# Optimization experiments

Measured on AMD Instinct MI355X. Metric: run time of the kernel, lower is better.

## Reference

```python
import jax, jax.numpy as jnp
import numpy as np

K = 16          # knn neighbors (init kwarg k)
GROUPS = 4      # GroupNorm groups
EPS = 1e-5
SLOPE = 0.2     # LeakyReLU negative slope


def fps(xyz, n):
    """Farthest point sampling. xyz: (B,N,3) -> idx (B,n). First index is 0 (pointnet2 convention)."""
    B, N, _ = xyz.shape

    def step(carry, _):
        dist, last = carry
        p = jnp.take_along_axis(xyz, last[:, None, None], axis=1)  # (B,1,3)
        d = jnp.sum((xyz - p) ** 2, axis=-1)                       # (B,N)
        dist = jnp.minimum(dist, d)
        nxt = jnp.argmax(dist, axis=-1).astype(jnp.int32)
        return (dist, nxt), nxt

    init = (jnp.full((B, N), jnp.inf, xyz.dtype), jnp.zeros((B,), jnp.int32))
    _, idxs = jax.lax.scan(step, init, None, length=n - 1)  # (n-1, B)
    return jnp.concatenate([jnp.zeros((B, 1), jnp.int32), idxs.T], axis=1)


def graph_feature(cq, fq, ck, fk):
    """DGCNN edge features. cq:(B,Q,3) fq:(B,Q,C) ck:(B,N,3) fk:(B,N,C) -> (B,Q,K,2C)."""
    d2 = (jnp.sum(cq * cq, -1)[:, :, None]
          - 2.0 * jnp.einsum('bqc,bnc->bqn', cq, ck)
          + jnp.sum(ck * ck, -1)[:, None, :])        # (B,Q,N)
    _, idx = jax.lax.top_k(-d2, K)                    # (B,Q,K) nearest first
    nb = jax.vmap(lambda f_, i_: f_[i_])(fk, idx)     # (B,Q,K,C)
    ctr = jnp.broadcast_to(fq[:, :, None, :], nb.shape)
    return jnp.concatenate([nb - ctr, ctr], axis=-1)


def conv_gn_lrelu(y, W, gw, gb):
    """1x1 Conv2d (no bias) + GroupNorm(4) + LeakyReLU(0.2). y: (B,Q,K,Cin), W: (Cout,Cin)."""
    y = jnp.einsum('bqkc,oc->bqko', y, W)
    B, Q, Kk, C = y.shape
    yg = y.reshape(B, Q * Kk, GROUPS, C // GROUPS)
    m = yg.mean(axis=(1, 3), keepdims=True)
    v = yg.var(axis=(1, 3), keepdims=True)
    y = ((yg - m) * jax.lax.rsqrt(v + EPS)).reshape(B, Q, Kk, C) * gw + gb
    return jnp.where(y > 0, y, SLOPE * y)


def setup_inputs() -> dict:
    key = jax.random.key(0)
    ks = jax.random.split(key, 16)
    B, N = 8, 4096
    s = lambda k_, shape, scale=0.1: (jax.random.normal(k_, shape, jnp.float32) * scale)
    return {
        'x': jax.random.normal(ks[0], (B, N, 7), jnp.float32),
        'W_in': s(ks[1], (8, 3), 0.5), 'b_in': s(ks[2], (8,), 0.02),
        'W1': s(ks[3], (32, 16), 0.2), 'g1w': jnp.ones((32,), jnp.float32), 'g1b': jnp.zeros((32,), jnp.float32),
        'W2': s(ks[4], (64, 64), 0.1), 'g2w': jnp.ones((64,), jnp.float32), 'g2b': jnp.zeros((64,), jnp.float32),
        'W3': s(ks[5], (64, 128), 0.1), 'g3w': jnp.ones((64,), jnp.float32), 'g3b': jnp.zeros((64,), jnp.float32),
        'W4': s(ks[6], (128, 128), 0.1), 'g4w': jnp.ones((128,), jnp.float32), 'g4b': jnp.zeros((128,), jnp.float32),
        'num0': 1024,
    }


def reference(x, W_in, b_in, W1, g1w, g1b, W2, g2w, g2b, W3, g3w, g3b, W4, g4w, g4b, num0):
    coor, normal, plane = x[..., :3], x[..., 3:6], x[..., 6:7]   # (B,N,3),(B,N,3),(B,N,1)

    # input_trans: Conv1d(3,8,1)
    f = jnp.einsum('bnc,oc->bno', coor, W_in) + b_in             # (B,N,8)

    g = graph_feature(coor, f, coor, f)                          # (B,N,K,16)
    f = conv_gn_lrelu(g, W1, g1w, g1b).max(axis=2)               # (B,N,32)

    idx = fps(coor, num0)
    gather = lambda a: jnp.take_along_axis(a, idx[:, :, None], axis=1)
    coor_q, normal_q, plane_q, f_q = gather(coor), gather(normal), gather(plane), gather(f)

    g = graph_feature(coor_q, f_q, coor, f)                      # (B,num0,K,64)
    f = conv_gn_lrelu(g, W2, g2w, g2b).max(axis=2)               # (B,num0,64)
    coor, normal, plane = coor_q, normal_q, plane_q

    g = graph_feature(coor, f, coor, f)                          # (B,num0,K,128)
    f = conv_gn_lrelu(g, W3, g3w, g3b).max(axis=2)               # (B,num0,64)

    idx = fps(coor, num0)  # source uses num[0] again
    gather = lambda a: jnp.take_along_axis(a, idx[:, :, None], axis=1)
    coor_q, normal_q, plane_q, f_q = gather(coor), gather(normal), gather(plane), gather(f)

    g = graph_feature(coor_q, f_q, coor, f)                      # (B,num0,K,128)
    f = conv_gn_lrelu(g, W4, g4w, g4b).max(axis=2)               # (B,num0,128)

    return coor_q, f, normal_q, plane_q
```

## Files before the change

kernel.cpp:

```cpp
#include <hip/hip_runtime.h>
#include <cstdint>

static constexpr int B   = 8;
static constexpr int N0  = 4096;
static constexpr int NQ  = 1024;
static constexpr int KNB = 16;

__device__ __forceinline__ unsigned long long wave_max_u64_l63(unsigned long long k) {
#define STEPU_(ctrl)                                                                    \
  {                                                                                     \
    unsigned lo_ = (unsigned)k, hi_ = (unsigned)(k >> 32);                              \
    unsigned plo_ = (unsigned)__builtin_amdgcn_update_dpp((int)lo_, (int)lo_, ctrl,     \
                                                          0xf, 0xf, false);             \
    unsigned phi_ = (unsigned)__builtin_amdgcn_update_dpp((int)hi_, (int)hi_, ctrl,     \
                                                          0xf, 0xf, false);             \
    unsigned long long pk_ = ((unsigned long long)phi_ << 32) | plo_;                   \
    if (pk_ > k) k = pk_;                                                               \
  }
  STEPU_(0x111) STEPU_(0x112) STEPU_(0x114) STEPU_(0x118) STEPU_(0x142) STEPU_(0x143)
#undef STEPU_
  return k;
}

__global__ void prep_kernel(const float* __restrict__ x,
                            const float* __restrict__ W_in,
                            const float* __restrict__ b_in,
                            const float* __restrict__ W1,
                            float4* __restrict__ c4, float* __restrict__ nrm,
                            float* __restrict__ pl, float* __restrict__ f0,
                            float* __restrict__ ctrY1) {
  int i = blockIdx.x * 256 + threadIdx.x;
  if (i >= B * N0) return;
  const float* xp = x + (size_t)i * 7;
  float cx = xp[0], cy = xp[1], cz = xp[2];
  float kk = __fadd_rn(__fadd_rn(__fmul_rn(cx, cx), __fmul_rn(cy, cy)), __fmul_rn(cz, cz));
  c4[i] = make_float4(cx, cy, cz, kk);
  nrm[i * 3 + 0] = xp[3]; nrm[i * 3 + 1] = xp[4]; nrm[i * 3 + 2] = xp[5];
  pl[i] = xp[6];
  float f[8];
#pragma unroll
  for (int o = 0; o < 8; o++) {
    f[o] = cx * W_in[o * 3 + 0] + cy * W_in[o * 3 + 1] + cz * W_in[o * 3 + 2] + b_in[o];
    f0[(size_t)i * 8 + o] = f[o];
  }
#pragma unroll
  for (int o = 0; o < 32; o++) {
    const float* wp = W1 + (size_t)o * 16 + 8;
    float acc = 0.f;
#pragma unroll
    for (int c = 0; c < 8; c++) acc = fmaf(f[c], wp[c], acc);
    ctrY1[(size_t)i * 32 + o] = acc;
  }
}

template <int NC>
__device__ __forceinline__ void knn_body(int bq, int lane,
                                         const float4* __restrict__ q4,
                                         const float4* __restrict__ k4,
                                         int Q, int Nk, int* __restrict__ out) {
  int b = bq / Q;
  float4 q = q4[bq];
  const float4* kb = k4 + (size_t)b * Nk + lane;
  const float INF    = __int_as_float(0x7f800000);
  const float NEGINF = __int_as_float(0xff800000);
  float myd = INF;
  int   myi = 0;
  float kth = INF;
  const bool isl0 = (lane & 15) == 0;
  constexpr int G = (NC >= 8) ? 8 : NC;
  for (int c0 = 0; c0 < NC; c0 += G) {
    float dg[G];
#pragma unroll
    for (int u = 0; u < G; u++) {
      float4 kp = kb[(c0 + u) * 64];
      float dot = __fadd_rn(__fadd_rn(__fmul_rn(q.x, kp.x), __fmul_rn(q.y, kp.y)),
                            __fmul_rn(q.z, kp.z));
      dg[u] = __fadd_rn(__fsub_rn(q.w, __fmul_rn(2.0f, dot)), kp.w);
    }
#pragma unroll
    for (int u = 0; u < G; u++) {
      float d = dg[u];
      unsigned long long m = __ballot(d < kth);
      while (m) {
        int j = __builtin_ctzll(m);
        float dv = __int_as_float(__builtin_amdgcn_readlane(__float_as_int(d), j));
        int   iv = (c0 + u) * 64 + j;
        bool gt = (myd > dv);
        float pd = __int_as_float(__builtin_amdgcn_update_dpp(
            0, __float_as_int(myd), 0x111, 0xf, 0xf, true));
        int   pi = __builtin_amdgcn_update_dpp(0, myi, 0x111, 0xf, 0xf, true);
        pd = isl0 ? NEGINF : pd;
        bool tp = (pd > dv);
        float nd = tp ? pd : dv;
        int   ni = tp ? pi : iv;
        myd = gt ? nd : myd;
        myi = gt ? ni : myi;
        kth = __int_as_float(__builtin_amdgcn_readlane(__float_as_int(myd), 15));
        m = __ballot(d < kth);
        m = (j < 63) ? (m & (~0ull << (j + 1))) : 0ull;
      }
    }
  }
  if (lane < KNB) out[(size_t)bq * KNB + lane] = myi;
}

template <int CF, int CO>
__device__ __forceinline__ void ctry_body(int i, int total, const float* __restrict__ fq,
                                          const float* __restrict__ W,
                                          float* __restrict__ ctrY,
                                          const int* __restrict__ ridx, int Q, int Nsrc) {
  if (i >= total) return;
  int o = i % CO, bq = i / CO;
  const float* fp;
  if (ridx) {
    int b = bq / Q;
    fp = fq + ((size_t)b * Nsrc + ridx[bq]) * CF;
  } else {
    fp = fq + (size_t)bq * CF;
  }
  const float* wp = W + (size_t)o * (2 * CF) + CF;
  float acc = 0.f;
#pragma unroll
  for (int c = 0; c < CF; c++) acc = fmaf(fp[c], wp[c], acc);
  ctrY[i] = acc;
}

template <int NPTS>
__device__ __forceinline__ void fps_body(const float4* __restrict__ cb, int* w) {
  constexpr int BLK = 256;
  constexpr int M = NPTS / BLK;
  constexpr int NW = BLK / 64;
  __shared__ __align__(16) float2 sxy[NPTS];
  __shared__ float szz[NPTS];
  __shared__ __align__(16) unsigned long long skey[2][NW];
  const int tid = threadIdx.x;
  const int wid = tid >> 6, lane = tid & 63;
  float cx[M], cy[M], cz[M], dist[M];
#pragma unroll
  for (int i = 0; i < M; i++) {
    float4 p = cb[tid * M + i];
    cx[i] = p.x; cy[i] = p.y; cz[i] = p.z;
    dist[i] = 3.4e38f;
    sxy[tid * M + i] = make_float2(p.x, p.y);
    szz[tid * M + i] = p.z;
  }
  w[0] = w[1] = w[2] = w[3] = 0;
  float4 p0 = cb[0];
  float px = p0.x, py = p0.y, pz = p0.z;
  __syncthreads();
  for (int t = 1; t < NQ; t++) {
    float bv = -1.f; int bi = 0;
#pragma unroll
    for (int i = 0; i < M; i++) {
      float dx = __fsub_rn(cx[i], px), dy = __fsub_rn(cy[i], py), dz = __fsub_rn(cz[i], pz);
      float d = __fadd_rn(__fadd_rn(__fmul_rn(dx, dx), __fmul_rn(dy, dy)), __fmul_rn(dz, dz));
      float dd = dist[i]; dd = (d < dd) ? d : dd; dist[i] = dd;
      if (dd > bv) { bv = dd; bi = tid * M + i; }
    }
    unsigned long long k =
        ((unsigned long long)__float_as_uint(bv) << 12) | (unsigned)(4095 - bi);
    k = wave_max_u64_l63(k);
    int p = t & 1;
    if (lane == 63) skey[p][wid] = k;
    __syncthreads();
    ulonglong2 ab = *(const ulonglong2*)&skey[p][0];
    ulonglong2 cd = *(const ulonglong2*)&skey[p][2];
    unsigned long long m0 = (ab.x > ab.y) ? ab.x : ab.y;
    unsigned long long m1 = (cd.x > cd.y) ? cd.x : cd.y;
    unsigned long long mk = (m0 > m1) ? m0 : m1;
    int win = 4095 - (int)(mk & 0xFFFull);
    float2 pxy = sxy[win];
    px = pxy.x; py = pxy.y; pz = szz[win];
    if (t == tid) w[0] = win;
    if (t == tid + 256) w[1] = win;
    if (t == tid + 512) w[2] = win;
    if (t == tid + 768) w[3] = win;
  }
}

template <int NC, int CF, int CO>
__device__ __forceinline__ void knnec_body(
    int blkid, const float4* __restrict__ q4, const float4* __restrict__ k4,
    const float* __restrict__ fq, const float* __restrict__ fk,
    const float* __restrict__ Wfull, const float* __restrict__ ctrY,
    const int* __restrict__ ridx,
    float* __restrict__ ymin, float* __restrict__ ymax,
    float* __restrict__ gstats, int Q, int Nk) {
  constexpr int J = CO / 4;
  constexpr int SEC = J * CF + 8;
  __shared__ float Wl[4 * SEC];
  __shared__ float sstat[8];
  for (int t = threadIdx.x; t < CO * CF; t += 256) {
    int o = t / CF, c = t % CF;
    Wl[(o / J) * SEC + (o % J) * CF + c] = Wfull[(size_t)o * (2 * CF) + c];
  }
  if (threadIdx.x < 8) sstat[threadIdx.x] = 0.0f;
  __syncthreads();
  const int wid = threadIdx.x >> 6, lane = threadIdx.x & 63;
  const int bq = blkid * 4 + wid;
  const int b = bq / Q;
  float4 q = q4[bq];
  const float4* kb = k4 + (size_t)b * Nk + lane;
  const float INF    = __int_as_float(0x7f800000);
  const float NEGINF = __int_as_float(0xff800000);
  float myd = INF;
  int   myi = 0;
  float kth = INF;
  const bool isl0 = (lane & 15) == 0;
  constexpr int G = (NC >= 8) ? 8 : NC;
  for (int c0 = 0; c0 < NC; c0 += G) {
    float dg[G];
#pragma unroll
    for (int u = 0; u < G; u++) {
      float4 kp = kb[(c0 + u) * 64];
      float dot = __fadd_rn(__fadd_rn(__fmul_rn(q.x, kp.x), __fmul_rn(q.y, kp.y)),
                            __fmul_rn(q.z, kp.z));
      dg[u] = __fadd_rn(__fsub_rn(q.w, __fmul_rn(2.0f, dot)), kp.w);
    }
#pragma unroll
    for (int u = 0; u < G; u++) {
      float d = dg[u];
      unsigned long long m = __ballot(d < kth);
      while (m) {
        int j = __builtin_ctzll(m);
        float dv = __int_as_float(__builtin_amdgcn_readlane(__float_as_int(d), j));
        int   iv = (c0 + u) * 64 + j;
        bool gt = (myd > dv);
        float pd = __int_as_float(__builtin_amdgcn_update_dpp(
            0, __float_as_int(myd), 0x111, 0xf, 0xf, true));
        int   pi = __builtin_amdgcn_update_dpp(0, myi, 0x111, 0xf, 0xf, true);
        pd = isl0 ? NEGINF : pd;
        bool tp = (pd > dv);
        float nd = tp ? pd : dv;
        int   nI = tp ? pi : iv;
        myd = gt ? nd : myd;
        myi = gt ? nI : myi;
        kth = __int_as_float(__builtin_amdgcn_readlane(__float_as_int(myd), 15));
        m = __ballot(d < kth);
        m = (j < 63) ? (m & (~0ull << (j + 1))) : 0ull;
      }
    }
  }
  const int g = lane >> 4, k = lane & 15;
  const int ni = myi;
  (void)k;
  const float* nbp = fk + (size_t)(b * Nk + ni) * CF;
  const float* cp = ridx ? fq + ((size_t)b * Nk + ridx[bq]) * CF
                         : fq + (size_t)bq * CF;
  float acc[J];
#pragma unroll
  for (int j = 0; j < J; j++) acc[j] = 0.0f;
  const float* wg = &Wl[g * SEC];
#pragma unroll
  for (int c = 0; c < CF; c += 4) {
    float4 nb4 = *(const float4*)(nbp + c);
    float4 c4  = *(const float4*)(cp + c);
    float e0 = nb4.x - c4.x, e1 = nb4.y - c4.y, e2 = nb4.z - c4.z, e3 = nb4.w - c4.w;
#pragma unroll
    for (int j = 0; j < J; j++) {
      float4 w4 = *(const float4*)(wg + j * CF + c);
      acc[j] = fmaf(e0, w4.x, acc[j]);
      acc[j] = fmaf(e1, w4.y, acc[j]);
      acc[j] = fmaf(e2, w4.z, acc[j]);
      acc[j] = fmaf(e3, w4.w, acc[j]);
    }
  }
  float s = 0.f, s2 = 0.f;
  const float* cyp = ctrY + (size_t)bq * CO + g * J;
#pragma unroll
  for (int j = 0; j < J; j++) {
    float y = acc[j] + cyp[j];
    acc[j] = y;
    s += y; s2 = fmaf(y, y, s2);
  }
  float mn[J];
#pragma unroll
  for (int j = 0; j < J; j++) mn[j] = acc[j];
#pragma unroll
  for (int m = 1; m < 16; m <<= 1) {
#pragma unroll
    for (int j = 0; j < J; j++) {
      float a = __shfl_xor(acc[j], m); if (a > acc[j]) acc[j] = a;
      float c2 = __shfl_xor(mn[j], m); if (c2 < mn[j]) mn[j] = c2;
    }
    s  += __shfl_xor(s, m);
    s2 += __shfl_xor(s2, m);
  }
  if ((lane & 15) == 0) {
    float* mnp = ymin + (size_t)bq * CO + g * J;
    float* mxp = ymax + (size_t)bq * CO + g * J;
#pragma unroll
    for (int j = 0; j < J; j++) { mnp[j] = mn[j]; mxp[j] = acc[j]; }
    atomicAdd(&sstat[g], s);
    atomicAdd(&sstat[4 + g], s2);
  }
  __syncthreads();
  if (threadIdx.x < 8) atomicAdd(&gstats[b * 8 + threadIdx.x], sstat[threadIdx.x]);
}

template <int CF, int CO>
__device__ __forceinline__ void edgeconv_body(
    int blkid, const float* __restrict__ fq, const float* __restrict__ fk,
    const int* __restrict__ knn, const float* __restrict__ Wfull,
    const float* __restrict__ ctrY, const int* __restrict__ ridx,
    float* __restrict__ ymin, float* __restrict__ ymax,
    float* __restrict__ gstats, int Q, int Nk) {
  constexpr int J = CO / 4;
  constexpr int SEC = J * CF + 8;
  __shared__ float Wl[4 * SEC];
  __shared__ float sstat[8];
  for (int t = threadIdx.x; t < CO * CF; t += 256) {
    int o = t / CF, c = t % CF;
    Wl[(o / J) * SEC + (o % J) * CF + c] = Wfull[(size_t)o * (2 * CF) + c];
  }
  if (threadIdx.x < 8) sstat[threadIdx.x] = 0.0f;
  __syncthreads();
  const int wid = threadIdx.x >> 6, lane = threadIdx.x & 63;
  const int bq = blkid * 4 + wid;
  const int b = bq / Q;
  const int g = lane >> 4, k = lane & 15;
  const int ni = knn[(size_t)bq * KNB + k];
  const float* nbp = fk + (size_t)(b * Nk + ni) * CF;
  const float* cp = ridx ? fq + ((size_t)b * Nk + ridx[bq]) * CF
                         : fq + (size_t)bq * CF;
  float acc[J];
#pragma unroll
  for (int j = 0; j < J; j++) acc[j] = 0.0f;
  const float* wg = &Wl[g * SEC];
#pragma unroll
  for (int c = 0; c < CF; c += 4) {
    float4 nb4 = *(const float4*)(nbp + c);
    float4 c4  = *(const float4*)(cp + c);
    float e0 = nb4.x - c4.x, e1 = nb4.y - c4.y, e2 = nb4.z - c4.z, e3 = nb4.w - c4.w;
#pragma unroll
    for (int j = 0; j < J; j++) {
      float4 w4 = *(const float4*)(wg + j * CF + c);
      acc[j] = fmaf(e0, w4.x, acc[j]);
      acc[j] = fmaf(e1, w4.y, acc[j]);
      acc[j] = fmaf(e2, w4.z, acc[j]);
      acc[j] = fmaf(e3, w4.w, acc[j]);
    }
  }
  float s = 0.f, s2 = 0.f;
  const float* cyp = ctrY + (size_t)bq * CO + g * J;
#pragma unroll
  for (int j = 0; j < J; j++) {
    float y = acc[j] + cyp[j];
    acc[j] = y;
    s += y; s2 = fmaf(y, y, s2);
  }
  float mn[J];
#pragma unroll
  for (int j = 0; j < J; j++) mn[j] = acc[j];
#pragma unroll
  for (int m = 1; m < 16; m <<= 1) {
#pragma unroll
    for (int j = 0; j < J; j++) {
      float a = __shfl_xor(acc[j], m); if (a > acc[j]) acc[j] = a;
      float c2 = __shfl_xor(mn[j], m); if (c2 < mn[j]) mn[j] = c2;
    }
    s  += __shfl_xor(s, m);
    s2 += __shfl_xor(s2, m);
  }
  if (k == 0) {
    float* mnp = ymin + (size_t)bq * CO + g * J;
    float* mxp = ymax + (size_t)bq * CO + g * J;
#pragma unroll
    for (int j = 0; j < J; j++) { mnp[j] = mn[j]; mxp[j] = acc[j]; }
    atomicAdd(&sstat[g], s);
    atomicAdd(&sstat[4 + g], s2);
  }
  __syncthreads();
  if (threadIdx.x < 8) atomicAdd(&gstats[b * 8 + threadIdx.x], sstat[threadIdx.x]);
}

__global__ __launch_bounds__(256, 2) void mega1_kernel(
    const float4* __restrict__ c40, const float* __restrict__ nrm,
    const float* __restrict__ pl, const float* __restrict__ f0,
    const float* __restrict__ W1, const float* __restrict__ ctrY1,
    int* __restrict__ idx1,
    float4* __restrict__ c4q1, float* __restrict__ nq1, float* __restrict__ pq1,
    float* __restrict__ ymin, float* __restrict__ ymax, float* __restrict__ gst1) {
  int blk = blockIdx.x;
  if (blk < 8) {
    const int b = blk, tid = threadIdx.x;
    const float4* cb = c40 + (size_t)b * N0;
    int w[4];
    fps_body<N0>(cb, w);
    int* idxb = idx1 + (size_t)b * NQ;
#pragma unroll
    for (int u = 0; u < 4; u++) {
      int r = tid + u * 256;
      int s = (u == 0 && tid == 0) ? 0 : w[u];
      idxb[r] = s;
      c4q1[(size_t)b * NQ + r] = cb[s];
      const float* np = nrm + ((size_t)b * N0 + s) * 3;
      float* ndp = nq1 + ((size_t)b * NQ + r) * 3;
      ndp[0] = np[0]; ndp[1] = np[1]; ndp[2] = np[2];
      pq1[(size_t)b * NQ + r] = pl[(size_t)b * N0 + s];
    }
  } else {
    knnec_body<64, 8, 32>(blk - 8, c40, c40, f0, f0, W1, ctrY1, nullptr,
                          ymin, ymax, gst1, N0, N0);
  }
}

__global__ __launch_bounds__(256, 2) void mega2_kernel(
    const float4* __restrict__ c40, const float4* __restrict__ c4q1,
    const float* __restrict__ nq1, const float* __restrict__ pq1,
    const float* __restrict__ f1, const int* __restrict__ idx1,
    const float* __restrict__ W2, const float* __restrict__ ctrY2,
    float* __restrict__ ymin, float* __restrict__ ymax, float* __restrict__ gst2,
    int* __restrict__ idx2, float4* __restrict__ c4q2,
    float* __restrict__ cq2out, float* __restrict__ nq2out,
    float* __restrict__ pq2out, int* __restrict__ knnB) {
  int blk = blockIdx.x;
  if (blk < 8) {
    const int b = blk, tid = threadIdx.x;
    const float4* cqb = c4q1 + (size_t)b * NQ;
    int w[4];
    fps_body<NQ>(cqb, w);
    int* idxb = idx2 + (size_t)b * NQ;
#pragma unroll
    for (int u = 0; u < 4; u++) {
      int r = tid + u * 256;
      int s = (u == 0 && tid == 0) ? 0 : w[u];
      idxb[r] = s;
      float4 c = cqb[s];
      c4q2[(size_t)b * NQ + r] = c;
      float* cd = cq2out + ((size_t)b * NQ + r) * 3;
      cd[0] = c.x; cd[1] = c.y; cd[2] = c.z;
      const float* np = nq1 + ((size_t)b * NQ + s) * 3;
      float* ndp = nq2out + ((size_t)b * NQ + r) * 3;
      ndp[0] = np[0]; ndp[1] = np[1]; ndp[2] = np[2];
      pq2out[(size_t)b * NQ + r] = pq1[(size_t)b * NQ + s];
    }
  } else if (blk < 8 + 2048) {
    knnec_body<64, 32, 64>(blk - 8, c4q1, c40, f1, f1, W2, ctrY2, idx1,
                           ymin, ymax, gst2, NQ, N0);
  } else {
    int bq = (blk - (8 + 2048)) * 4 + (threadIdx.x >> 6);
    knn_body<16>(bq, threadIdx.x & 63, c4q1, c4q1, NQ, NQ, knnB);
  }
}

__global__ __launch_bounds__(256) void mega3_kernel(
    const float4* __restrict__ c4q1, const float4* __restrict__ c4q2,
    const float* __restrict__ f3, const int* __restrict__ idx2,
    const float* __restrict__ W4, const float* __restrict__ ctrY4,
    float* __restrict__ ymin, float* __restrict__ ymax, float* __restrict__ gst4) {
  knnec_body<16, 64, 128>(blockIdx.x, c4q2, c4q1, f3, f3, W4, ctrY4, idx2,
                          ymin, ymax, gst4, NQ, NQ);
}

template <int CF, int CO>
__global__ void ctry_kernel(const float* __restrict__ fq, const float* __restrict__ W,
                            float* __restrict__ ctrY, int total,
                            const int* __restrict__ ridx, int Q, int Nsrc) {
  int i = blockIdx.x * 256 + threadIdx.x;
  ctry_body<CF, CO>(i, total, fq, W, ctrY, ridx, Q, Nsrc);
}

template <int CF, int CO>
__global__ __launch_bounds__(256) void edgeconv_kernel(
    const float* __restrict__ fq, const float* __restrict__ fk,
    const int* __restrict__ knn, const float* __restrict__ Wfull,
    const float* __restrict__ ctrY, const int* __restrict__ ridx,
    float* __restrict__ ymin, float* __restrict__ ymax,
    float* __restrict__ gstats, int Q, int Nk) {
  edgeconv_body<CF, CO>(blockIdx.x, fq, fk, knn, Wfull, ctrY, ridx,
                        ymin, ymax, gstats, Q, Nk);
}

template <int CO>
__global__ void gn_out_kernel(const float* __restrict__ ymin, const float* __restrict__ ymax,
                              const float* __restrict__ gstats, const float* __restrict__ gw,
                              const float* __restrict__ gb, float* __restrict__ fout,
                              int total, int Q, float inv_cnt) {
  int i = blockIdx.x * 256 + threadIdx.x;
  if (i >= total) return;
  constexpr int J = CO / 4;
  int o = i % CO; int bq = i / CO; int b = bq / Q;
  int g = o / J;
  float m  = gstats[b * 8 + g] * inv_cnt;
  float s2 = gstats[b * 8 + 4 + g] * inv_cnt;
  float rs = rsqrtf(s2 - m * m + 1e-5f);
  float sc = gw[o] * rs;
  float sel = (sc >= 0.f) ? ymax[i] : ymin[i];
  float v = (sel - m) * sc + gb[o];
  fout[i] = (v > 0.f) ? v : 0.2f * v;
}

extern "C" void kernel_launch(void* const* d_in, const int* in_sizes, int n_in,
                              void* d_out, int out_size, void* d_ws, size_t ws_size,
                              hipStream_t stream) {
  (void)in_sizes; (void)n_in; (void)out_size; (void)ws_size;
  const float* x    = (const float*)d_in[0];
  const float* W_in = (const float*)d_in[1];
  const float* b_in = (const float*)d_in[2];
  const float* W1   = (const float*)d_in[3];
  const float* g1w  = (const float*)d_in[4];
  const float* g1b  = (const float*)d_in[5];
  const float* W2   = (const float*)d_in[6];
  const float* g2w  = (const float*)d_in[7];
  const float* g2b  = (const float*)d_in[8];
  const float* W3   = (const float*)d_in[9];
  const float* g3w  = (const float*)d_in[10];
  const float* g3b  = (const float*)d_in[11];
  const float* W4   = (const float*)d_in[12];
  const float* g4w  = (const float*)d_in[13];
  const float* g4b  = (const float*)d_in[14];

  float* ws = (float*)d_ws;
  size_t o_c40  = 0;
  size_t o_nrm  = o_c40  + (size_t)B * N0 * 4;
  size_t o_pl   = o_nrm  + (size_t)B * N0 * 3;
  size_t o_f0   = o_pl   + (size_t)B * N0;
  size_t o_f1   = o_f0   + (size_t)B * N0 * 8;
  size_t o_ctrY = o_f1   + (size_t)B * N0 * 32;
  size_t o_ymin = o_ctrY + (size_t)B * N0 * 32;
  size_t o_ymax = o_ymin + (size_t)B * N0 * 32;
  size_t o_knnB = o_ymax + (size_t)B * N0 * 32;
  size_t o_gst  = o_knnB + (size_t)B * NQ * KNB;
  size_t o_idx1 = o_gst  + 4 * B * 8;
  size_t o_idx2 = o_idx1 + (size_t)B * NQ;
  size_t o_c4q1 = o_idx2 + (size_t)B * NQ;
  size_t o_c4q2 = o_c4q1 + (size_t)B * NQ * 4;
  size_t o_nq1  = o_c4q2 + (size_t)B * NQ * 4;
  size_t o_pq1  = o_nq1  + (size_t)B * NQ * 3;
  size_t o_f2   = o_pq1  + (size_t)B * NQ;
  size_t o_f3   = o_f2   + (size_t)B * NQ * 64;

  float4* c40  = (float4*)(ws + o_c40);
  float*  nrm  = ws + o_nrm;   float* pl   = ws + o_pl;
  float*  f0   = ws + o_f0;    float* f1   = ws + o_f1;
  float*  ctrY = ws + o_ctrY;  float* ymin = ws + o_ymin;  float* ymax = ws + o_ymax;
  int*    knnB = (int*)(ws + o_knnB);
  float*  gst  = ws + o_gst;
  int*    idx1 = (int*)(ws + o_idx1);
  int*    idx2 = (int*)(ws + o_idx2);
  float4* c4q1 = (float4*)(ws + o_c4q1);
  float4* c4q2 = (float4*)(ws + o_c4q2);
  float*  nq1  = ws + o_nq1;   float* pq1  = ws + o_pq1;
  float*  f2   = ws + o_f2;    float* f3   = ws + o_f3;

  float* out  = (float*)d_out;
  float* cq2  = out;
  float* fout = out + (size_t)B * NQ * 3;
  float* nq2  = fout + (size_t)B * NQ * 128;
  float* pq2  = nq2 + (size_t)B * NQ * 3;

  hipMemsetAsync(gst, 0, 4 * B * 8 * sizeof(float), stream);

  prep_kernel<<<(B * N0 + 255) / 256, 256, 0, stream>>>(x, W_in, b_in, W1,
                                                        c40, nrm, pl, f0, ctrY);

  mega1_kernel<<<8 + 8192, 256, 0, stream>>>(c40, nrm, pl, f0, W1, ctrY,
                                             idx1, c4q1, nq1, pq1,
                                             ymin, ymax, gst + 0);
  gn_out_kernel<32><<<(B * N0 * 32 + 255) / 256, 256, 0, stream>>>(
      ymin, ymax, gst + 0, g1w, g1b, f1, B * N0 * 32, N0, 1.0f / (4096.0f * 16.0f * 8.0f));
  ctry_kernel<32, 64><<<(B * NQ * 64 + 255) / 256, 256, 0, stream>>>(
      f1, W2, ctrY, B * NQ * 64, idx1, NQ, N0);

  mega2_kernel<<<8 + 2048 + 2048, 256, 0, stream>>>(
      c40, c4q1, nq1, pq1, f1, idx1, W2, ctrY, ymin, ymax, gst + B * 8,
      idx2, c4q2, cq2, nq2, pq2, knnB);
  gn_out_kernel<64><<<(B * NQ * 64 + 255) / 256, 256, 0, stream>>>(
      ymin, ymax, gst + B * 8, g2w, g2b, f2, B * NQ * 64, NQ, 1.0f / (1024.0f * 16.0f * 16.0f));

  ctry_kernel<64, 64><<<(B * NQ * 64 + 255) / 256, 256, 0, stream>>>(
      f2, W3, ctrY, B * NQ * 64, nullptr, 0, 0);
  edgeconv_kernel<64, 64><<<B * NQ / 4, 256, 0, stream>>>(f2, f2, knnB, W3, ctrY, nullptr,
                                                          ymin, ymax, gst + 2 * B * 8, NQ, NQ);
  gn_out_kernel<64><<<(B * NQ * 64 + 255) / 256, 256, 0, stream>>>(
      ymin, ymax, gst + 2 * B * 8, g3w, g3b, f3, B * NQ * 64, NQ, 1.0f / (1024.0f * 16.0f * 16.0f));

  ctry_kernel<64, 128><<<(B * NQ * 128 + 255) / 256, 256, 0, stream>>>(
      f3, W4, ctrY, B * NQ * 128, idx2, NQ, NQ);
  mega3_kernel<<<B * NQ / 4, 256, 0, stream>>>(c4q1, c4q2, f3, idx2, W4, ctrY,
                                               ymin, ymax, gst + 3 * B * 8);
  gn_out_kernel<128><<<(B * NQ * 128 + 255) / 256, 256, 0, stream>>>(
      ymin, ymax, gst + 3 * B * 8, g4w, g4b, fout, B * NQ * 128, NQ, 1.0f / (1024.0f * 16.0f * 32.0f));
}
```

Measured before the change: 1.460 ms.

## Fuse GroupNorm apply and center projection into downstream edge-conv kernels

```diff
diff --git a/kernel.cpp b/kernel.cpp
--- a/kernel.cpp
+++ b/kernel.cpp
@@ -20,6 +20,12 @@
   STEPU_(0x111) STEPU_(0x112) STEPU_(0x114) STEPU_(0x118) STEPU_(0x142) STEPU_(0x143)
 #undef STEPU_
   return k;
+}
+
+__device__ __forceinline__ float gnf(float mx, float mn, float scv, float mo, float gb) {
+  float sel = (scv >= 0.f) ? mx : mn;
+  float v = (sel - mo) * scv + gb;
+  return (v > 0.f) ? v : 0.2f * v;
 }
 
 __global__ void prep_kernel(const float* __restrict__ x,
@@ -80,9 +86,9 @@
 #pragma unroll
     for (int u = 0; u < G; u++) {
       float d = dg[u];
-      unsigned long long m = __ballot(d < kth);
-      while (m) {
-        int j = __builtin_ctzll(m);
+      unsigned long long msk = __ballot(d < kth);
+      while (msk) {
+        int j = __builtin_ctzll(msk);
         float dv = __int_as_float(__builtin_amdgcn_readlane(__float_as_int(d), j));
         int   iv = (c0 + u) * 64 + j;
         bool gt = (myd > dv);
@@ -96,33 +102,12 @@
         myd = gt ? nd : myd;
         myi = gt ? ni : myi;
         kth = __int_as_float(__builtin_amdgcn_readlane(__float_as_int(myd), 15));
-        m = __ballot(d < kth);
-        m = (j < 63) ? (m & (~0ull << (j + 1))) : 0ull;
+        msk = __ballot(d < kth);
+        msk = (j < 63) ? (msk & (~0ull << (j + 1))) : 0ull;
       }
     }
   }
   if (lane < KNB) out[(size_t)bq * KNB + lane] = myi;
-}
-
-template <int CF, int CO>
-__device__ __forceinline__ void ctry_body(int i, int total, const float* __restrict__ fq,
-                                          const float* __restrict__ W,
-                                          float* __restrict__ ctrY,
-                                          const int* __restrict__ ridx, int Q, int Nsrc) {
-  if (i >= total) return;
-  int o = i % CO, bq = i / CO;
-  const float* fp;
-  if (ridx) {
-    int b = bq / Q;
-    fp = fq + ((size_t)b * Nsrc + ridx[bq]) * CF;
-  } else {
-    fp = fq + (size_t)bq * CF;
-  }
-  const float* wp = W + (size_t)o * (2 * CF) + CF;
-  float acc = 0.f;
-#pragma unroll
-  for (int c = 0; c < CF; c++) acc = fmaf(fp[c], wp[c], acc);
-  ctrY[i] = acc;
 }
 
 template <int NPTS>
@@ -220,9 +205,9 @@
 #pragma unroll
     for (int u = 0; u < G; u++) {
       float d = dg[u];
-      unsigned long long m = __ballot(d < kth);
-      while (m) {
-        int j = __builtin_ctzll(m);
+      unsigned long long msk = __ballot(d < kth);
+      while (msk) {
+        int j = __builtin_ctzll(msk);
         float dv = __int_as_float(__builtin_amdgcn_readlane(__float_as_int(d), j));
         int   iv = (c0 + u) * 64 + j;
         bool gt = (myd > dv);
@@ -236,14 +221,13 @@
         myd = gt ? nd : myd;
         myi = gt ? nI : myi;
         kth = __int_as_float(__builtin_amdgcn_readlane(__float_as_int(myd), 15));
-        m = __ballot(d < kth);
-        m = (j < 63) ? (m & (~0ull << (j + 1))) : 0ull;
+        msk = __ballot(d < kth);
+        msk = (j < 63) ? (msk & (~0ull << (j + 1))) : 0ull;
       }
     }
   }
-  const int g = lane >> 4, k = lane & 15;
+  const int g = lane >> 4;
   const int ni = myi;
-  (void)k;
   const float* nbp = fk + (size_t)(b * Nk + ni) * CF;
   const float* cp = ridx ? fq + ((size_t)b * Nk + ridx[bq]) * CF
                          : fq + (size_t)bq * CF;
@@ -298,40 +282,121 @@
   if (threadIdx.x < 8) atomicAdd(&gstats[b * 8 + threadIdx.x], sstat[threadIdx.x]);
 }
 
-template <int CF, int CO>
-__device__ __forceinline__ void edgeconv_body(
-    int blkid, const float* __restrict__ fq, const float* __restrict__ fk,
-    const int* __restrict__ knn, const float* __restrict__ Wfull,
-    const float* __restrict__ ctrY, const int* __restrict__ ridx,
+template <int NC, int CF, int CO, bool HAS_KNN>
+__device__ __forceinline__ void ec_gn_core(
+    int blkid, const float4* __restrict__ q4, const float4* __restrict__ k4,
+    const int* __restrict__ knn,
+    const float* __restrict__ yminP, const float* __restrict__ ymaxP,
+    const float* __restrict__ gstP, const float* __restrict__ gwP,
+    const float* __restrict__ gbP, float invP,
+    const float* __restrict__ Wfull, const int* __restrict__ ridx,
     float* __restrict__ ymin, float* __restrict__ ymax,
     float* __restrict__ gstats, int Q, int Nk) {
   constexpr int J = CO / 4;
   constexpr int SEC = J * CF + 8;
   __shared__ float Wl[4 * SEC];
   __shared__ float sstat[8];
+  __shared__ __align__(16) float t_scv[CF];
+  __shared__ __align__(16) float t_mo[CF];
+  __shared__ __align__(16) float t_gb[CF];
+  __shared__ __align__(16) float wfc[4][CF];
+  __shared__ float scy[4][CO];
+  const int b = (blkid * 4) / Q;
   for (int t = threadIdx.x; t < CO * CF; t += 256) {
     int o = t / CF, c = t % CF;
     Wl[(o / J) * SEC + (o % J) * CF + c] = Wfull[(size_t)o * (2 * CF) + c];
+  }
+  if (threadIdx.x < CF) {
+    int c = threadIdx.x;
+    int gg = c / (CF / 4);
+    float m  = gstP[b * 8 + gg] * invP;
+    float s2 = gstP[b * 8 + 4 + gg] * invP;
+    float rs = rsqrtf(s2 - m * m + 1e-5f);
+    t_scv[c] = gwP[c] * rs;
+    t_mo[c]  = m;
+    t_gb[c]  = gbP[c];
   }
   if (threadIdx.x < 8) sstat[threadIdx.x] = 0.0f;
   __syncthreads();
   const int wid = threadIdx.x >> 6, lane = threadIdx.x & 63;
   const int bq = blkid * 4 + wid;
-  const int b = bq / Q;
-  const int g = lane >> 4, k = lane & 15;
-  const int ni = knn[(size_t)bq * KNB + k];
-  const float* nbp = fk + (size_t)(b * Nk + ni) * CF;
-  const float* cp = ridx ? fq + ((size_t)b * Nk + ridx[bq]) * CF
-                         : fq + (size_t)bq * CF;
+  size_t cbase = (ridx ? ((size_t)b * Nk + ridx[bq]) : (size_t)bq) * CF;
+  if (lane < CF)
+    wfc[wid][lane] = gnf(ymaxP[cbase + lane], yminP[cbase + lane],
+                         t_scv[lane], t_mo[lane], t_gb[lane]);
+  for (int oo = lane; oo < CO; oo += 64) {
+    const float* wp = Wfull + (size_t)oo * (2 * CF) + CF;
+    float acc0 = 0.f;
+#pragma unroll
+    for (int c = 0; c < CF; c++) acc0 = fmaf(wfc[wid][c], wp[c], acc0);
+    scy[wid][oo] = acc0;
+  }
+  int ni;
+  if (HAS_KNN) {
+    float4 q = q4[bq];
+    const float4* kb = k4 + (size_t)b * Nk + lane;
+    const float INF    = __int_as_float(0x7f800000);
+    const float NEGINF = __int_as_float(0xff800000);
+    float myd = INF;
+    int   myi = 0;
+    float kth = INF;
+    const bool isl0 = (lane & 15) == 0;
+    constexpr int G = (NC >= 8) ? 8 : NC;
+    for (int c0 = 0; c0 < NC; c0 += G) {
+      float dg[G];
+#pragma unroll
+      for (int u = 0; u < G; u++) {
+        float4 kp = kb[(c0 + u) * 64];
+        float dot = __fadd_rn(__fadd_rn(__fmul_rn(q.x, kp.x), __fmul_rn(q.y, kp.y)),
+                              __fmul_rn(q.z, kp.z));
+        dg[u] = __fadd_rn(__fsub_rn(q.w, __fmul_rn(2.0f, dot)), kp.w);
+      }
+#pragma unroll
+      for (int u = 0; u < G; u++) {
+        float d = dg[u];
+        unsigned long long msk = __ballot(d < kth);
+        while (msk) {
+          int j = __builtin_ctzll(msk);
+          float dv = __int_as_float(__builtin_amdgcn_readlane(__float_as_int(d), j));
+          int   iv = (c0 + u) * 64 + j;
+          bool gt = (myd > dv);
+          float pd = __int_as_float(__builtin_amdgcn_update_dpp(
+              0, __float_as_int(myd), 0x111, 0xf, 0xf, true));
+          int   pi = __builtin_amdgcn_update_dpp(0, myi, 0x111, 0xf, 0xf, true);
+          pd = isl0 ? NEGINF : pd;
+          bool tp = (pd > dv);
+          float nd = tp ? pd : dv;
+          int   nI = tp ? pi : iv;
+          myd = gt ? nd : myd;
+          myi = gt ? nI : myi;
+          kth = __int_as_float(__builtin_amdgcn_readlane(__float_as_int(myd), 15));
+          msk = __ballot(d < kth);
+          msk = (j < 63) ? (msk & (~0ull << (j + 1))) : 0ull;
+        }
+      }
+    }
+    ni = myi;
+  } else {
+    ni = knn[(size_t)bq * KNB + (lane & 15)];
+  }
+  const int g = lane >> 4;
+  size_t nbase = ((size_t)b * Nk + ni) * CF;
   float acc[J];
 #pragma unroll
   for (int j = 0; j < J; j++) acc[j] = 0.0f;
   const float* wg = &Wl[g * SEC];
 #pragma unroll
   for (int c = 0; c < CF; c += 4) {
-    float4 nb4 = *(const float4*)(nbp + c);
-    float4 c4  = *(const float4*)(cp + c);
-    float e0 = nb4.x - c4.x, e1 = nb4.y - c4.y, e2 = nb4.z - c4.z, e3 = nb4.w - c4.w;
+    float4 mx4 = *(const float4*)(ymaxP + nbase + c);
+    float4 mn4 = *(const float4*)(yminP + nbase + c);
+    float4 sc4 = *(const float4*)(&t_scv[c]);
+    float4 mo4 = *(const float4*)(&t_mo[c]);
+    float4 gb4 = *(const float4*)(&t_gb[c]);
+    float4 c4  = *(const float4*)(&wfc[wid][c]);
+    float e0 = gnf(mx4.x, mn4.x, sc4.x, mo4.x, gb4.x) - c4.x;
+    float e1 = gnf(mx4.y, mn4.y, sc4.y, mo4.y, gb4.y) - c4.y;
+    float e2 = gnf(mx4.z, mn4.z, sc4.z, mo4.z, gb4.z) - c4.z;
+    float e3 = gnf(mx4.w, mn4.w, sc4.w, mo4.w, gb4.w) - c4.w;
 #pragma unroll
     for (int j = 0; j < J; j++) {
       float4 w4 = *(const float4*)(wg + j * CF + c);
@@ -342,10 +407,9 @@
     }
   }
   float s = 0.f, s2 = 0.f;
-  const float* cyp = ctrY + (size_t)bq * CO + g * J;
 #pragma unroll
   for (int j = 0; j < J; j++) {
-    float y = acc[j] + cyp[j];
+    float y = acc[j] + scy[wid][g * J + j];
     acc[j] = y;
     s += y; s2 = fmaf(y, y, s2);
   }
@@ -362,7 +426,7 @@
     s  += __shfl_xor(s, m);
     s2 += __shfl_xor(s2, m);
   }
-  if (k == 0) {
+  if ((lane & 15) == 0) {
     float* mnp = ymin + (size_t)bq * CO + g * J;
     float* mxp = ymax + (size_t)bq * CO + g * J;
 #pragma unroll
@@ -408,9 +472,11 @@
 __global__ __launch_bounds__(256, 2) void mega2_kernel(
     const float4* __restrict__ c40, const float4* __restrict__ c4q1,
     const float* __restrict__ nq1, const float* __restrict__ pq1,
-    const float* __restrict__ f1, const int* __restrict__ idx1,
-    const float* __restrict__ W2, const float* __restrict__ ctrY2,
-    float* __restrict__ ymin, float* __restrict__ ymax, float* __restrict__ gst2,
+    const float* __restrict__ yminA, const float* __restrict__ ymaxA,
+    const float* __restrict__ gst1, const float* __restrict__ g1w,
+    const float* __restrict__ g1b, float inv1,
+    const int* __restrict__ idx1, const float* __restrict__ W2,
+    float* __restrict__ yminB, float* __restrict__ ymaxB, float* __restrict__ gst2,
     int* __restrict__ idx2, float4* __restrict__ c4q2,
     float* __restrict__ cq2out, float* __restrict__ nq2out,
     float* __restrict__ pq2out, int* __restrict__ knnB) {
@@ -436,40 +502,37 @@
       pq2out[(size_t)b * NQ + r] = pq1[(size_t)b * NQ + s];
     }
   } else if (blk < 8 + 2048) {
-    knnec_body<64, 32, 64>(blk - 8, c4q1, c40, f1, f1, W2, ctrY2, idx1,
-                           ymin, ymax, gst2, NQ, N0);
+    ec_gn_core<64, 32, 64, true>(blk - 8, c4q1, c40, nullptr,
+                                 yminA, ymaxA, gst1, g1w, g1b, inv1,
+                                 W2, idx1, yminB, ymaxB, gst2, NQ, N0);
   } else {
     int bq = (blk - (8 + 2048)) * 4 + (threadIdx.x >> 6);
     knn_body<16>(bq, threadIdx.x & 63, c4q1, c4q1, NQ, NQ, knnB);
   }
 }
 
-__global__ __launch_bounds__(256) void mega3_kernel(
+__global__ __launch_bounds__(256) void ec3g_kernel(
+    const int* __restrict__ knnB,
+    const float* __restrict__ yminB, const float* __restrict__ ymaxB,
+    const float* __restrict__ gst2, const float* __restrict__ g2w,
+    const float* __restrict__ g2b, float inv2,
+    const float* __restrict__ W3,
+    float* __restrict__ yminC, float* __restrict__ ymaxC, float* __restrict__ gst3) {
+  ec_gn_core<16, 64, 64, false>(blockIdx.x, nullptr, nullptr, knnB,
+                                yminB, ymaxB, gst2, g2w, g2b, inv2,
+                                W3, nullptr, yminC, ymaxC, gst3, NQ, NQ);
+}
+
+__global__ __launch_bounds__(256) void mega3g_kernel(
     const float4* __restrict__ c4q1, const float4* __restrict__ c4q2,
-    const float* __restrict__ f3, const int* __restrict__ idx2,
-    const float* __restrict__ W4, const float* __restrict__ ctrY4,
-    float* __restrict__ ymin, float* __restrict__ ymax, float* __restrict__ gst4) {
-  knnec_body<16, 64, 128>(blockIdx.x, c4q2, c4q1, f3, f3, W4, ctrY4, idx2,
-                          ymin, ymax, gst4, NQ, NQ);
-}
-
-template <int CF, int CO>
-__global__ void ctry_kernel(const float* __restrict__ fq, const float* __restrict__ W,
-                            float* __restrict__ ctrY, int total,
-                            const int* __restrict__ ridx, int Q, int Nsrc) {
-  int i = blockIdx.x * 256 + threadIdx.x;
-  ctry_body<CF, CO>(i, total, fq, W, ctrY, ridx, Q, Nsrc);
-}
-
-template <int CF, int CO>
-__global__ __launch_bounds__(256) void edgeconv_kernel(
-    const float* __restrict__ fq, const float* __restrict__ fk,
-    const int* __restrict__ knn, const float* __restrict__ Wfull,
-    const float* __restrict__ ctrY, const int* __restrict__ ridx,
-    float* __restrict__ ymin, float* __restrict__ ymax,
-    float* __restrict__ gstats, int Q, int Nk) {
-  edgeconv_body<CF, CO>(blockIdx.x, fq, fk, knn, Wfull, ctrY, ridx,
-                        ymin, ymax, gstats, Q, Nk);
+    const float* __restrict__ yminC, const float* __restrict__ ymaxC,
+    const float* __restrict__ gst3, const float* __restrict__ g3w,
+    const float* __restrict__ g3b, float inv3,
+    const int* __restrict__ idx2, const float* __restrict__ W4,
+    float* __restrict__ yminD, float* __restrict__ ymaxD, float* __restrict__ gst4) {
+  ec_gn_core<16, 64, 128, true>(blockIdx.x, c4q2, c4q1, nullptr,
+                                yminC, ymaxC, gst3, g3w, g3b, inv3,
+                                W4, idx2, yminD, ymaxD, gst4, NQ, NQ);
 }
 
 template <int CO>
@@ -512,37 +575,41 @@
   const float* g4b  = (const float*)d_in[14];
 
   float* ws = (float*)d_ws;
-  size_t o_c40  = 0;
-  size_t o_nrm  = o_c40  + (size_t)B * N0 * 4;
-  size_t o_pl   = o_nrm  + (size_t)B * N0 * 3;
-  size_t o_f0   = o_pl   + (size_t)B * N0;
-  size_t o_f1   = o_f0   + (size_t)B * N0 * 8;
-  size_t o_ctrY = o_f1   + (size_t)B * N0 * 32;
-  size_t o_ymin = o_ctrY + (size_t)B * N0 * 32;
-  size_t o_ymax = o_ymin + (size_t)B * N0 * 32;
-  size_t o_knnB = o_ymax + (size_t)B * N0 * 32;
-  size_t o_gst  = o_knnB + (size_t)B * NQ * KNB;
-  size_t o_idx1 = o_gst  + 4 * B * 8;
-  size_t o_idx2 = o_idx1 + (size_t)B * NQ;
-  size_t o_c4q1 = o_idx2 + (size_t)B * NQ;
-  size_t o_c4q2 = o_c4q1 + (size_t)B * NQ * 4;
-  size_t o_nq1  = o_c4q2 + (size_t)B * NQ * 4;
-  size_t o_pq1  = o_nq1  + (size_t)B * NQ * 3;
-  size_t o_f2   = o_pq1  + (size_t)B * NQ;
-  size_t o_f3   = o_f2   + (size_t)B * NQ * 64;
-
-  float4* c40  = (float4*)(ws + o_c40);
-  float*  nrm  = ws + o_nrm;   float* pl   = ws + o_pl;
-  float*  f0   = ws + o_f0;    float* f1   = ws + o_f1;
-  float*  ctrY = ws + o_ctrY;  float* ymin = ws + o_ymin;  float* ymax = ws + o_ymax;
-  int*    knnB = (int*)(ws + o_knnB);
-  float*  gst  = ws + o_gst;
-  int*    idx1 = (int*)(ws + o_idx1);
-  int*    idx2 = (int*)(ws + o_idx2);
-  float4* c4q1 = (float4*)(ws + o_c4q1);
-  float4* c4q2 = (float4*)(ws + o_c4q2);
-  float*  nq1  = ws + o_nq1;   float* pq1  = ws + o_pq1;
-  float*  f2   = ws + o_f2;    float* f3   = ws + o_f3;
+  size_t o_c40   = 0;
+  size_t o_nrm   = o_c40   + (size_t)B * N0 * 4;
+  size_t o_pl    = o_nrm   + (size_t)B * N0 * 3;
+  size_t o_f0    = o_pl    + (size_t)B * N0;
+  size_t o_ctrY1 = o_f0    + (size_t)B * N0 * 8;
+  size_t o_yAmin = o_ctrY1 + (size_t)B * N0 * 32;
+  size_t o_yAmax = o_yAmin + (size_t)B * N0 * 32;
+  size_t o_yBmin = o_yAmax + (size_t)B * N0 * 32;
+  size_t o_yBmax = o_yBmin + (size_t)B * NQ * 64;
+  size_t o_yCmin = o_yBmax + (size_t)B * NQ * 64;
+  size_t o_yCmax = o_yCmin + (size_t)B * NQ * 64;
+  size_t o_knnB  = o_yCmax + (size_t)B * NQ * 64;
+  size_t o_gst   = o_knnB  + (size_t)B * NQ * KNB;
+  size_t o_idx1  = o_gst   + 4 * B * 8;
+  size_t o_idx2  = o_idx1  + (size_t)B * NQ;
+  size_t o_c4q1  = o_idx2  + (size_t)B * NQ;
+  size_t o_c4q2  = o_c4q1  + (size_t)B * NQ * 4;
+  size_t o_nq1   = o_c4q2  + (size_t)B * NQ * 4;
+  size_t o_pq1   = o_nq1   + (size_t)B * NQ * 3;
+
+  float4* c40   = (float4*)(ws + o_c40);
+  float*  nrm   = ws + o_nrm;    float* pl    = ws + o_pl;
+  float*  f0    = ws + o_f0;     float* ctrY1 = ws + o_ctrY1;
+  float*  yAmin = ws + o_yAmin;  float* yAmax = ws + o_yAmax;
+  float*  yBmin = ws + o_yBmin;  float* yBmax = ws + o_yBmax;
+  float*  yCmin = ws + o_yCmin;  float* yCmax = ws + o_yCmax;
+  float*  yDmin = ctrY1;
+  float*  yDmax = yAmin;
+  int*    knnB  = (int*)(ws + o_knnB);
+  float*  gst   = ws + o_gst;
+  int*    idx1  = (int*)(ws + o_idx1);
+  int*    idx2  = (int*)(ws + o_idx2);
+  float4* c4q1  = (float4*)(ws + o_c4q1);
+  float4* c4q2  = (float4*)(ws + o_c4q2);
+  float*  nq1   = ws + o_nq1;    float* pq1   = ws + o_pq1;
 
   float* out  = (float*)d_out;
   float* cq2  = out;
@@ -550,36 +617,33 @@
   float* nq2  = fout + (size_t)B * NQ * 128;
   float* pq2  = nq2 + (size_t)B * NQ * 3;
 
+  const float inv1 = 1.0f / (4096.0f * 16.0f * 8.0f);
+  const float inv2 = 1.0f / (1024.0f * 16.0f * 16.0f);
+  const float inv3 = 1.0f / (1024.0f * 16.0f * 16.0f);
+  const float inv4 = 1.0f / (1024.0f * 16.0f * 32.0f);
+
   hipMemsetAsync(gst, 0, 4 * B * 8 * sizeof(float), stream);
 
   prep_kernel<<<(B * N0 + 255) / 256, 256, 0, stream>>>(x, W_in, b_in, W1,
-                                                        c40, nrm, pl, f0, ctrY);
-
-  mega1_kernel<<<8 + 8192, 256, 0, stream>>>(c40, nrm, pl, f0, W1, ctrY,
+                                                        c40, nrm, pl, f0, ctrY1);
+
+  mega1_kernel<<<8 + 8192, 256, 0, stream>>>(c40, nrm, pl, f0, W1, ctrY1,
                                              idx1, c4q1, nq1, pq1,
-                                             ymin, ymax, gst + 0);
-  gn_out_kernel<32><<<(B * N0 * 32 + 255) / 256, 256, 0, stream>>>(
-      ymin, ymax, gst + 0, g1w, g1b, f1, B * N0 * 32, N0, 1.0f / (4096.0f * 16.0f * 8.0f));
-  ctry_kernel<32, 64><<<(B * NQ * 64 + 255) / 256, 256, 0, stream>>>(
-      f1, W2, ctrY, B * NQ * 64, idx1, NQ, N0);
+                                             yAmin, yAmax, gst + 0);
 
   mega2_kernel<<<8 + 2048 + 2048, 256, 0, stream>>>(
-      c40, c4q1, nq1, pq1, f1, idx1, W2, ctrY, ymin, ymax, gst + B * 8,
+      c40, c4q1, nq1, pq1, yAmin, yAmax, gst + 0, g1w, g1b, inv1,
+      idx1, W2, yBmin, yBmax, gst + B * 8,
       idx2, c4q2, cq2, nq2, pq2, knnB);
-  gn_out_kernel<64><<<(B * NQ * 64 + 255) / 256, 256, 0, stream>>>(
-      ymin, ymax, gst + B * 8, g2w, g2b, f2, B * NQ * 64, NQ, 1.0f / (1024.0f * 16.0f * 16.0f));
-
-  ctry_kernel<64, 64><<<(B * NQ * 64 + 255) / 256, 256, 0, stream>>>(
-      f2, W3, ctrY, B * NQ * 64, nullptr, 0, 0);
-  edgeconv_kernel<64, 64><<<B * NQ / 4, 256, 0, stream>>>(f2, f2, knnB, W3, ctrY, nullptr,
-                                                          ymin, ymax, gst + 2 * B * 8, NQ, NQ);
-  gn_out_kernel<64><<<(B * NQ * 64 + 255) / 256, 256, 0, stream>>>(
-      ymin, ymax, gst + 2 * B * 8, g3w, g3b, f3, B * NQ * 64, NQ, 1.0f / (1024.0f * 16.0f * 16.0f));
-
-  ctry_kernel<64, 128><<<(B * NQ * 128 + 255) / 256, 256, 0, stream>>>(
-      f3, W4, ctrY, B * NQ * 128, idx2, NQ, NQ);
-  mega3_kernel<<<B * NQ / 4, 256, 0, stream>>>(c4q1, c4q2, f3, idx2, W4, ctrY,
-                                               ymin, ymax, gst + 3 * B * 8);
+
+  ec3g_kernel<<<B * NQ / 4, 256, 0, stream>>>(
+      knnB, yBmin, yBmax, gst + B * 8, g2w, g2b, inv2, W3,
+      yCmin, yCmax, gst + 2 * B * 8);
+
+  mega3g_kernel<<<B * NQ / 4, 256, 0, stream>>>(
+      c4q1, c4q2, yCmin, yCmax, gst + 2 * B * 8, g3w, g3b, inv3,
+      idx2, W4, yDmin, yDmax, gst + 3 * B * 8);
+
   gn_out_kernel<128><<<(B * NQ * 128 + 255) / 256, 256, 0, stream>>>(
-      ymin, ymax, gst + 3 * B * 8, g4w, g4b, fout, B * NQ * 128, NQ, 1.0f / (1024.0f * 16.0f * 32.0f));
-}
+      yDmin, yDmax, gst + 3 * B * 8, g4w, g4b, fout, B * NQ * 128, NQ, inv4);
+}
```

Result: no change. 1.438 ms, median of 2 (-1.5%).
